# Performance work log

Measured on AMD Instinct MI355X. Metric: run time of the kernel, lower is better.

## Reference

```python
import jax, jax.numpy as jnp
import numpy as np

NUM_HEADS = 12
HEAD_DIM = 64  # d_out // num_heads = 768 // 12


def setup_inputs() -> dict:
    key = jax.random.key(0)
    k1, k2 = jax.random.split(key)
    x = jax.random.normal(k1, (2, 2048, 768), dtype=jnp.float32)
    # torch Linear weight: [d_out, d_in], y = x @ W.T
    Wq = jax.random.normal(k2, (768, 768), dtype=jnp.float32) * 0.02
    return {"x": x, "Wq": Wq}


def reference(x, Wq):
    b, n, d_in = x.shape
    H, hd = NUM_HEADS, HEAD_DIM
    d_out = H * hd
    # NOTE: the original module uses Wq for queries, keys AND values.
    qkv = x @ Wq.T                                   # [b, n, d_out]
    h = qkv.reshape(b, n, H, hd).transpose(0, 2, 1, 3)  # [b, H, n, hd]
    scores = jnp.einsum('bhqd,bhkd->bhqk', h, h)      # [b, H, n, n]
    causal = jnp.triu(jnp.ones((n, n), dtype=bool), k=1)
    scores = jnp.where(causal, -jnp.inf, scores)
    attn = jax.nn.softmax(scores / jnp.sqrt(jnp.float32(hd)), axis=-1)
    ctx = jnp.einsum('bhqk,bhkd->bhqd', attn, h)      # [b, H, n, hd]
    # faithful to source: transpose(-2,-1) -> [b, H, hd, n], then view(b, n, d_out)
    ctx = ctx.transpose(0, 1, 3, 2)
    return ctx.reshape(b, n, d_out)
```

## Files before the change

### kernel.cpp

```cpp
#include <hip/hip_runtime.h>
#include <math.h>

typedef __attribute__((ext_vector_type(8))) short  short8;
typedef __attribute__((ext_vector_type(4))) float  floatx4;
typedef __attribute__((ext_vector_type(4))) unsigned short ushort4v;

#define MFMA16(a, b, c) __builtin_amdgcn_mfma_f32_16x16x32_bf16(a, b, c, 0, 0, 0)

constexpr int NSEQ = 2048;
constexpr int DIN  = 768;
constexpr int NH   = 12;
constexpr size_t NX = (size_t)2 * NSEQ * DIN;
constexpr size_t NW = (size_t)DIN * DIN;
constexpr float QSCALE = 0.18033688011112042f;

__device__ __forceinline__ ushort f2bf(float f) {
    unsigned u = __float_as_uint(f);
    u += 0x7FFF + ((u >> 16) & 1);
    return (ushort)(u >> 16);
}
__device__ __forceinline__ float bf2f(ushort u) {
    return __uint_as_float(((unsigned)u) << 16);
}

__global__ __launch_bounds__(256)
void cvt_bf16(const float* __restrict__ x, const float* __restrict__ Wq,
              ushort* __restrict__ dst)
{
    size_t i = ((size_t)blockIdx.x * 256 + threadIdx.x) * 8;
    const float* s = (i < NX) ? (x + i) : (Wq + (i - NX));
    float4 f0 = ((const float4*)s)[0];
    float4 f1 = ((const float4*)s)[1];
    short8 o;
    o[0] = (short)f2bf(f0.x); o[1] = (short)f2bf(f0.y);
    o[2] = (short)f2bf(f0.z); o[3] = (short)f2bf(f0.w);
    o[4] = (short)f2bf(f1.x); o[5] = (short)f2bf(f1.y);
    o[6] = (short)f2bf(f1.z); o[7] = (short)f2bf(f1.w);
    *(short8*)(dst + i) = o;
}

__global__ __launch_bounds__(256, 3)
void qkv_mfma(const ushort* __restrict__ xb, const ushort* __restrict__ wb,
              ushort* __restrict__ h)
{
    __shared__ ushort As[64 * 72];
    __shared__ ushort Bs[128 * 72];

    const int tid  = threadIdx.x;
    const int w    = tid >> 6;
    const int lane = tid & 63;
    const int m    = lane & 15;
    const int quad = lane >> 4;
    const int r0   = blockIdx.x * 64;
    const int c0   = blockIdx.y * 128;
    const int mrow0 = (w & 1) * 32;
    const int ncol0 = (w >> 1) * 64;

    floatx4 C[2][4] = {};
    short8 ar[2], br[4];

    #pragma unroll
    for (int i = 0; i < 2; ++i) {
        int id = tid + i * 256;
        ar[i] = *(const short8*)(xb + (size_t)(r0 + (id >> 3)) * DIN + (id & 7) * 8);
    }
    #pragma unroll
    for (int i = 0; i < 4; ++i) {
        int id = tid + i * 256;
        br[i] = *(const short8*)(wb + (size_t)(c0 + (id >> 3)) * DIN + (id & 7) * 8);
    }

    for (int kk = 0; kk < 12; ++kk) {
        __syncthreads();
        #pragma unroll
        for (int i = 0; i < 2; ++i) {
            int id = tid + i * 256;
            *(short8*)&As[(id >> 3) * 72 + (id & 7) * 8] = ar[i];
        }
        #pragma unroll
        for (int i = 0; i < 4; ++i) {
            int id = tid + i * 256;
            *(short8*)&Bs[(id >> 3) * 72 + (id & 7) * 8] = br[i];
        }
        if (kk < 11) {
            const int k0 = (kk + 1) * 64;
            #pragma unroll
            for (int i = 0; i < 2; ++i) {
                int id = tid + i * 256;
                ar[i] = *(const short8*)(xb + (size_t)(r0 + (id >> 3)) * DIN + k0 + (id & 7) * 8);
            }
            #pragma unroll
            for (int i = 0; i < 4; ++i) {
                int id = tid + i * 256;
                br[i] = *(const short8*)(wb + (size_t)(c0 + (id >> 3)) * DIN + k0 + (id & 7) * 8);
            }
        }
        __syncthreads();

        #pragma unroll
        for (int kt2 = 0; kt2 < 2; ++kt2) {
            short8 a0 = *(const short8*)&As[(mrow0 + m)      * 72 + kt2 * 32 + quad * 8];
            short8 a1 = *(const short8*)&As[(mrow0 + 16 + m) * 72 + kt2 * 32 + quad * 8];
            #pragma unroll
            for (int nt = 0; nt < 4; ++nt) {
                short8 bf = *(const short8*)&Bs[(ncol0 + nt * 16 + m) * 72 + kt2 * 32 + quad * 8];
                C[0][nt] = MFMA16(a0, bf, C[0][nt]);
                C[1][nt] = MFMA16(a1, bf, C[1][nt]);
            }
        }
    }

    #pragma unroll
    for (int mt = 0; mt < 2; ++mt)
        #pragma unroll
        for (int nt = 0; nt < 4; ++nt) {
            int cg = c0 + ncol0 + nt * 16 + m;
            int head = cg >> 6, d = cg & 63;
            #pragma unroll
            for (int r = 0; r < 4; ++r) {
                int rg = r0 + mrow0 + mt * 16 + quad * 4 + r;
                int b = rg >> 11, q = rg & 2047;
                h[((size_t)(b * NH + head) * NSEQ + q) * 64 + d] = f2bf(C[mt][nt][r]);
            }
        }
}

__global__ __launch_bounds__(256, 4)
void attn_mfma(const ushort* __restrict__ h, float* __restrict__ out)
{
    __shared__ ushort Ks[64 * 72];
    __shared__ ushort Vt[64 * 72];
    __shared__ ushort Ps[4 * 16 * 72];

    const int tid  = threadIdx.x;
    const int w    = tid >> 6;
    const int lane = tid & 63;
    const int m    = lane & 15;
    const int quad = lane >> 4;

    const int qt = 31 - blockIdx.x;
    const int bh = blockIdx.y;
    const int q0 = qt * 64;
    const int wq = q0 + w * 16;
    const ushort* __restrict__ Hh = h + (size_t)bh * NSEQ * 64;

    short8 qa[2];
    #pragma unroll
    for (int kt2 = 0; kt2 < 2; ++kt2) {
        short8 raw = *(const short8*)(Hh + (size_t)(wq + m) * 64 + kt2 * 32 + quad * 8);
        #pragma unroll
        for (int j = 0; j < 8; ++j)
            qa[kt2][j] = (short)f2bf(bf2f((ushort)raw[j]) * QSCALE);
    }

    floatx4 O[4] = {};
    float lacc = 0.0f;
    ushort* Psw = Ps + w * 16 * 72;

    const int kr2  = (tid & 31) * 2;
    const int part = tid >> 5;
    const int nkt  = qt + 1;

    short8 a0, a1;
    {
        const ushort* src = Hh + (size_t)kr2 * 64 + part * 8;
        a0 = *(const short8*)src;
        a1 = *(const short8*)(src + 64);
    }

    for (int kt = 0; kt < nkt; ++kt) {
        __syncthreads();
        union { short8 v; ushort u[8]; } ua, ub;
        ua.v = a0; ub.v = a1;
        *(short8*)&Ks[kr2       * 72 + part * 8] = a0;
        *(short8*)&Ks[(kr2 + 1) * 72 + part * 8] = a1;
        #pragma unroll
        for (int i = 0; i < 8; ++i) {
            unsigned pk = (unsigned)ua.u[i] | ((unsigned)ub.u[i] << 16);
            *(unsigned*)&Vt[(part * 8 + i) * 72 + kr2] = pk;
        }
        if (kt + 1 < nkt) {
            const ushort* src = Hh + (size_t)((kt + 1) * 64 + kr2) * 64 + part * 8;
            a0 = *(const short8*)src;
            a1 = *(const short8*)(src + 64);
        }
        __syncthreads();

        floatx4 S[4] = {};
        #pragma unroll
        for (int kt2 = 0; kt2 < 2; ++kt2)
            #pragma unroll
            for (int mt = 0; mt < 4; ++mt) {
                short8 ka = *(const short8*)&Ks[(mt * 16 + m) * 72 + kt2 * 32 + quad * 8];
                S[mt] = MFMA16(ka, qa[kt2], S[mt]);
            }

        const int k0 = kt * 64;
        if (kt == nkt - 1) {
            #pragma unroll
            for (int mt = 0; mt < 4; ++mt) {
                ushort4v pw;
                #pragma unroll
                for (int r = 0; r < 4; ++r) {
                    int kg = k0 + mt * 16 + quad * 4 + r;
                    float p = (kg <= wq + m) ? exp2f(S[mt][r]) : 0.0f;
                    lacc += p;
                    pw[r] = f2bf(p);
                }
                *(ushort4v*)&Psw[m * 72 + mt * 16 + quad * 4] = pw;
            }
        } else {
            #pragma unroll
            for (int mt = 0; mt < 4; ++mt) {
                ushort4v pw;
                #pragma unroll
                for (int r = 0; r < 4; ++r) {
                    float p = exp2f(S[mt][r]);
                    lacc += p;
                    pw[r] = f2bf(p);
                }
                *(ushort4v*)&Psw[m * 72 + mt * 16 + quad * 4] = pw;
            }
        }

        #pragma unroll
        for (int kt2 = 0; kt2 < 2; ++kt2) {
            short8 pb = *(const short8*)&Psw[m * 72 + kt2 * 32 + quad * 8];
            #pragma unroll
            for (int mt = 0; mt < 4; ++mt) {
                short8 va = *(const short8*)&Vt[(mt * 16 + m) * 72 + kt2 * 32 + quad * 8];
                O[mt] = MFMA16(va, pb, O[mt]);
            }
        }
    }

    lacc += __shfl_xor(lacc, 16);
    lacc += __shfl_xor(lacc, 32);
    float linv = 1.0f / lacc;

    #pragma unroll
    for (int mt = 0; mt < 4; ++mt)
        #pragma unroll
        for (int r = 0; r < 4; ++r) {
            int d = mt * 16 + quad * 4 + r;
            out[((size_t)bh * 64 + d) * NSEQ + q0 + w * 16 + m] = O[mt][r] * linv;
        }
}

extern "C" void kernel_launch(void* const* d_in, const int* in_sizes, int n_in,
                              void* d_out, int out_size, void* d_ws, size_t ws_size,
                              hipStream_t stream)
{
    (void)in_sizes; (void)n_in; (void)out_size; (void)ws_size;
    const float* x  = (const float*)d_in[0];
    const float* Wq = (const float*)d_in[1];
    float* out = (float*)d_out;

    ushort* xb = (ushort*)d_ws;
    ushort* wb = xb + NX;
    ushort* hb = wb + NW;

    cvt_bf16<<<dim3((NX + NW) / (8 * 256)), dim3(256), 0, stream>>>(x, Wq, xb);
    qkv_mfma<<<dim3(64, 6), dim3(256), 0, stream>>>(xb, wb, hb);
    attn_mfma<<<dim3(32, 24), dim3(256), 0, stream>>>(hb, out);
}
```

Before: 132.1 us.

## Fuse bf16 conversion into QKV GEMM and split attention KV across chunks

Removes the standalone fp32-to-bf16 conversion kernel; the projection GEMM now loads fp32 x and Wq and converts while staging into shared memory. Attention is split along the key dimension into chunks of up to 8 tiles, giving a balanced grid of 80 blocks per head, with partial outputs written to a workspace and summed by a new combine kernel. The row-sum is computed by an extra MFMA against a ones row appended to V, and exp2 and bf16 packing use hardware intrinsics. The cost is extra partial-buffer traffic, a third launch, and more fp32 global reads in the GEMM.

```diff
diff --git a/kernel.cpp b/kernel.cpp
--- a/kernel.cpp
+++ b/kernel.cpp
@@ -1,18 +1,18 @@
 #include <hip/hip_runtime.h>
+#include <hip/hip_bf16.h>
 #include <math.h>
 
 typedef __attribute__((ext_vector_type(8))) short  short8;
 typedef __attribute__((ext_vector_type(4))) float  floatx4;
-typedef __attribute__((ext_vector_type(4))) unsigned short ushort4v;
 
 #define MFMA16(a, b, c) __builtin_amdgcn_mfma_f32_16x16x32_bf16(a, b, c, 0, 0, 0)
 
 constexpr int NSEQ = 2048;
 constexpr int DIN  = 768;
 constexpr int NH   = 12;
-constexpr size_t NX = (size_t)2 * NSEQ * DIN;
-constexpr size_t NW = (size_t)DIN * DIN;
 constexpr float QSCALE = 0.18033688011112042f;
+constexpr int PART_STRIDE = 64 * 64 + 64;
+constexpr size_t HB_ELEMS = (size_t)2 * NH * NSEQ * 64;
 
 __device__ __forceinline__ ushort f2bf(float f) {
     unsigned u = __float_as_uint(f);
@@ -22,25 +22,19 @@
 __device__ __forceinline__ float bf2f(ushort u) {
     return __uint_as_float(((unsigned)u) << 16);
 }
-
-__global__ __launch_bounds__(256)
-void cvt_bf16(const float* __restrict__ x, const float* __restrict__ Wq,
-              ushort* __restrict__ dst)
-{
-    size_t i = ((size_t)blockIdx.x * 256 + threadIdx.x) * 8;
-    const float* s = (i < NX) ? (x + i) : (Wq + (i - NX));
-    float4 f0 = ((const float4*)s)[0];
-    float4 f1 = ((const float4*)s)[1];
-    short8 o;
-    o[0] = (short)f2bf(f0.x); o[1] = (short)f2bf(f0.y);
-    o[2] = (short)f2bf(f0.z); o[3] = (short)f2bf(f0.w);
-    o[4] = (short)f2bf(f1.x); o[5] = (short)f2bf(f1.y);
-    o[6] = (short)f2bf(f1.z); o[7] = (short)f2bf(f1.w);
-    *(short8*)(dst + i) = o;
+__device__ __forceinline__ unsigned pk2(float a, float b) {
+    __hip_bfloat162 h = __float22bfloat162_rn(float2{a, b});
+    return *(unsigned*)&h;
+}
+__device__ __forceinline__ short8 cvt8(float4 a, float4 b) {
+    union { short8 s; unsigned u[4]; } r;
+    r.u[0] = pk2(a.x, a.y); r.u[1] = pk2(a.z, a.w);
+    r.u[2] = pk2(b.x, b.y); r.u[3] = pk2(b.z, b.w);
+    return r.s;
 }
 
 __global__ __launch_bounds__(256, 3)
-void qkv_mfma(const ushort* __restrict__ xb, const ushort* __restrict__ wb,
+void qkv_mfma(const float* __restrict__ x, const float* __restrict__ Wq,
               ushort* __restrict__ h)
 {
     __shared__ ushort As[64 * 72];
@@ -56,44 +50,34 @@
     const int mrow0 = (w & 1) * 32;
     const int ncol0 = (w >> 1) * 64;
 
+    const int xr = tid >> 2, xc = (tid & 3) * 16;
+    const int wr = tid >> 1, wc = (tid & 1) * 32;
+
     floatx4 C[2][4] = {};
-    short8 ar[2], br[4];
-
-    #pragma unroll
-    for (int i = 0; i < 2; ++i) {
-        int id = tid + i * 256;
-        ar[i] = *(const short8*)(xb + (size_t)(r0 + (id >> 3)) * DIN + (id & 7) * 8);
-    }
-    #pragma unroll
-    for (int i = 0; i < 4; ++i) {
-        int id = tid + i * 256;
-        br[i] = *(const short8*)(wb + (size_t)(c0 + (id >> 3)) * DIN + (id & 7) * 8);
-    }
+    float4 xa[4], wa[8];
+
+    #pragma unroll
+    for (int j = 0; j < 4; ++j)
+        xa[j] = *(const float4*)(x + (size_t)(r0 + xr) * DIN + xc + j * 4);
+    #pragma unroll
+    for (int j = 0; j < 8; ++j)
+        wa[j] = *(const float4*)(Wq + (size_t)(c0 + wr) * DIN + wc + j * 4);
 
     for (int kk = 0; kk < 12; ++kk) {
         __syncthreads();
-        #pragma unroll
-        for (int i = 0; i < 2; ++i) {
-            int id = tid + i * 256;
-            *(short8*)&As[(id >> 3) * 72 + (id & 7) * 8] = ar[i];
-        }
-        #pragma unroll
-        for (int i = 0; i < 4; ++i) {
-            int id = tid + i * 256;
-            *(short8*)&Bs[(id >> 3) * 72 + (id & 7) * 8] = br[i];
-        }
+        *(short8*)&As[xr * 72 + xc]     = cvt8(xa[0], xa[1]);
+        *(short8*)&As[xr * 72 + xc + 8] = cvt8(xa[2], xa[3]);
+        #pragma unroll
+        for (int v = 0; v < 4; ++v)
+            *(short8*)&Bs[wr * 72 + wc + v * 8] = cvt8(wa[v * 2], wa[v * 2 + 1]);
         if (kk < 11) {
             const int k0 = (kk + 1) * 64;
             #pragma unroll
-            for (int i = 0; i < 2; ++i) {
-                int id = tid + i * 256;
-                ar[i] = *(const short8*)(xb + (size_t)(r0 + (id >> 3)) * DIN + k0 + (id & 7) * 8);
-            }
-            #pragma unroll
-            for (int i = 0; i < 4; ++i) {
-                int id = tid + i * 256;
-                br[i] = *(const short8*)(wb + (size_t)(c0 + (id >> 3)) * DIN + k0 + (id & 7) * 8);
-            }
+            for (int j = 0; j < 4; ++j)
+                xa[j] = *(const float4*)(x + (size_t)(r0 + xr) * DIN + k0 + xc + j * 4);
+            #pragma unroll
+            for (int j = 0; j < 8; ++j)
+                wa[j] = *(const float4*)(Wq + (size_t)(c0 + wr) * DIN + k0 + wc + j * 4);
         }
         __syncthreads();
 
@@ -126,10 +110,11 @@
 }
 
 __global__ __launch_bounds__(256, 4)
-void attn_mfma(const ushort* __restrict__ h, float* __restrict__ out)
+void attn_mfma(const ushort* __restrict__ h, float* __restrict__ parts,
+               float* __restrict__ out)
 {
     __shared__ ushort Ks[64 * 72];
-    __shared__ ushort Vt[64 * 72];
+    __shared__ ushort Vt[80 * 72];
     __shared__ ushort Ps[4 * 16 * 72];
 
     const int tid  = threadIdx.x;
@@ -138,11 +123,21 @@
     const int m    = lane & 15;
     const int quad = lane >> 4;
 
-    const int qt = 31 - blockIdx.x;
+    const int u  = blockIdx.x;
     const int bh = blockIdx.y;
-    const int q0 = qt * 64;
-    const int wq = q0 + w * 16;
+    int qt, kc;
+    if (u < 32)      { qt = 24 + (u >> 2); kc = u & 3; }
+    else if (u < 56) { int v = u - 32; int q3 = v / 3; qt = 16 + q3; kc = v - q3 * 3; }
+    else if (u < 72) { int v = u - 56; qt = 8 + (v >> 1); kc = v & 1; }
+    else             { qt = u - 72; kc = 0; }
+    const int nc  = (qt + 8) >> 3;
+    const int kt0 = kc * 8;
+    const int kt1 = min(kc * 8 + 8, qt + 1);
+    const int q0  = qt * 64;
+    const int wq  = q0 + w * 16;
     const ushort* __restrict__ Hh = h + (size_t)bh * NSEQ * 64;
+
+    if (tid < 32) ((unsigned*)&Vt[64 * 72])[tid] = 0x3F803F80u;
 
     short8 qa[2];
     #pragma unroll
@@ -154,21 +149,20 @@
     }
 
     floatx4 O[4] = {};
-    float lacc = 0.0f;
+    floatx4 O5 = {};
     ushort* Psw = Ps + w * 16 * 72;
 
     const int kr2  = (tid & 31) * 2;
     const int part = tid >> 5;
-    const int nkt  = qt + 1;
 
     short8 a0, a1;
     {
-        const ushort* src = Hh + (size_t)kr2 * 64 + part * 8;
+        const ushort* src = Hh + (size_t)(kt0 * 64 + kr2) * 64 + part * 8;
         a0 = *(const short8*)src;
         a1 = *(const short8*)(src + 64);
     }
 
-    for (int kt = 0; kt < nkt; ++kt) {
+    for (int kt = kt0; kt < kt1; ++kt) {
         __syncthreads();
         union { short8 v; ushort u[8]; } ua, ub;
         ua.v = a0; ub.v = a1;
@@ -179,7 +173,7 @@
             unsigned pk = (unsigned)ua.u[i] | ((unsigned)ub.u[i] << 16);
             *(unsigned*)&Vt[(part * 8 + i) * 72 + kr2] = pk;
         }
-        if (kt + 1 < nkt) {
+        if (kt + 1 < kt1) {
             const ushort* src = Hh + (size_t)((kt + 1) * 64 + kr2) * 64 + part * 8;
             a0 = *(const short8*)src;
             a1 = *(const short8*)(src + 64);
@@ -195,31 +189,28 @@
                 S[mt] = MFMA16(ka, qa[kt2], S[mt]);
             }
 
-        const int k0 = kt * 64;
-        if (kt == nkt - 1) {
+        const int kb = kt * 64;
+        if (kt == qt) {
             #pragma unroll
             for (int mt = 0; mt < 4; ++mt) {
-                ushort4v pw;
+                float p[4];
                 #pragma unroll
                 for (int r = 0; r < 4; ++r) {
-                    int kg = k0 + mt * 16 + quad * 4 + r;
-                    float p = (kg <= wq + m) ? exp2f(S[mt][r]) : 0.0f;
-                    lacc += p;
-                    pw[r] = f2bf(p);
+                    int kg = kb + mt * 16 + quad * 4 + r;
+                    p[r] = (kg <= wq + m) ? __builtin_amdgcn_exp2f(S[mt][r]) : 0.0f;
                 }
-                *(ushort4v*)&Psw[m * 72 + mt * 16 + quad * 4] = pw;
+                uint2 pw = {pk2(p[0], p[1]), pk2(p[2], p[3])};
+                *(uint2*)&Psw[m * 72 + mt * 16 + quad * 4] = pw;
             }
         } else {
             #pragma unroll
             for (int mt = 0; mt < 4; ++mt) {
-                ushort4v pw;
+                float p[4];
                 #pragma unroll
-                for (int r = 0; r < 4; ++r) {
-                    float p = exp2f(S[mt][r]);
-                    lacc += p;
-                    pw[r] = f2bf(p);
-                }
-                *(ushort4v*)&Psw[m * 72 + mt * 16 + quad * 4] = pw;
+                for (int r = 0; r < 4; ++r)
+                    p[r] = __builtin_amdgcn_exp2f(S[mt][r]);
+                uint2 pw = {pk2(p[0], p[1]), pk2(p[2], p[3])};
+                *(uint2*)&Psw[m * 72 + mt * 16 + quad * 4] = pw;
             }
         }
 
@@ -231,20 +222,69 @@
                 short8 va = *(const short8*)&Vt[(mt * 16 + m) * 72 + kt2 * 32 + quad * 8];
                 O[mt] = MFMA16(va, pb, O[mt]);
             }
-        }
-    }
-
-    lacc += __shfl_xor(lacc, 16);
-    lacc += __shfl_xor(lacc, 32);
-    float linv = 1.0f / lacc;
-
-    #pragma unroll
-    for (int mt = 0; mt < 4; ++mt)
-        #pragma unroll
-        for (int r = 0; r < 4; ++r) {
-            int d = mt * 16 + quad * 4 + r;
-            out[((size_t)bh * 64 + d) * NSEQ + q0 + w * 16 + m] = O[mt][r] * linv;
-        }
+            short8 v5 = *(const short8*)&Vt[(64 + m) * 72 + kt2 * 32 + quad * 8];
+            O5 = MFMA16(v5, pb, O5);
+        }
+    }
+
+    float lval = __shfl(O5[0], m);
+
+    if (nc == 1) {
+        float linv = 1.0f / lval;
+        #pragma unroll
+        for (int mt = 0; mt < 4; ++mt)
+            #pragma unroll
+            for (int r = 0; r < 4; ++r) {
+                int d = mt * 16 + quad * 4 + r;
+                out[((size_t)bh * 64 + d) * NSEQ + q0 + w * 16 + m] = O[mt][r] * linv;
+            }
+    } else {
+        float* P = parts + (size_t)((bh * 32 + qt) * 4 + kc) * PART_STRIDE;
+        #pragma unroll
+        for (int mt = 0; mt < 4; ++mt)
+            #pragma unroll
+            for (int r = 0; r < 4; ++r)
+                P[(mt * 16 + quad * 4 + r) * 64 + w * 16 + m] = O[mt][r];
+        if (quad == 0) P[4096 + w * 16 + m] = O5[0];
+    }
+}
+
+__global__ __launch_bounds__(256)
+void combine(const float* __restrict__ parts, float* __restrict__ out)
+{
+    const int qt = 8 + blockIdx.x;
+    const int bh = blockIdx.y;
+    const int nc = (qt + 8) >> 3;
+    const float* base = parts + (size_t)((bh * 32 + qt) * 4) * PART_STRIDE;
+
+    __shared__ float linv[64];
+    const int tid = threadIdx.x;
+    if (tid < 64) {
+        float s = 0.0f;
+        for (int c = 0; c < nc; ++c) s += base[c * PART_STRIDE + 4096 + tid];
+        linv[tid] = 1.0f / s;
+    }
+    __syncthreads();
+
+    const int d  = tid >> 2;
+    const int qo = (tid & 3) * 16;
+    float4 acc[4] = {};
+    for (int c = 0; c < nc; ++c) {
+        const float4* p = (const float4*)(base + c * PART_STRIDE + d * 64 + qo);
+        #pragma unroll
+        for (int j = 0; j < 4; ++j) {
+            float4 v = p[j];
+            acc[j].x += v.x; acc[j].y += v.y; acc[j].z += v.z; acc[j].w += v.w;
+        }
+    }
+    float* dst = out + ((size_t)bh * 64 + d) * NSEQ + qt * 64 + qo;
+    #pragma unroll
+    for (int j = 0; j < 4; ++j) {
+        float4 lv = *(const float4*)&linv[qo + j * 4];
+        float4 o = make_float4(acc[j].x * lv.x, acc[j].y * lv.y,
+                               acc[j].z * lv.z, acc[j].w * lv.w);
+        *(float4*)(dst + j * 4) = o;
+    }
 }
 
 extern "C" void kernel_launch(void* const* d_in, const int* in_sizes, int n_in,
@@ -256,11 +296,10 @@
     const float* Wq = (const float*)d_in[1];
     float* out = (float*)d_out;
 
-    ushort* xb = (ushort*)d_ws;
-    ushort* wb = xb + NX;
-    ushort* hb = wb + NW;
-
-    cvt_bf16<<<dim3((NX + NW) / (8 * 256)), dim3(256), 0, stream>>>(x, Wq, xb);
-    qkv_mfma<<<dim3(64, 6), dim3(256), 0, stream>>>(xb, wb, hb);
-    attn_mfma<<<dim3(32, 24), dim3(256), 0, stream>>>(hb, out);
-}
+    ushort* hb    = (ushort*)d_ws;
+    float*  partb = (float*)((char*)d_ws + HB_ELEMS * sizeof(ushort));
+
+    qkv_mfma<<<dim3(64, 6),  dim3(256), 0, stream>>>(x, Wq, hb);
+    attn_mfma<<<dim3(80, 24), dim3(256), 0, stream>>>(hb, partb, out);
+    combine<<<dim3(24, 24),  dim3(256), 0, stream>>>(partb, out);
+}
```

Measured after the change: 136.7 us. 3.5% more time.

## Pair causal query tiles per block, drop LDS from GEMM, fold row-sum into MFMA

Applied to the files above, without the earlier changes.

The attention kernel now gives each block two query tiles (p and 31-p), which balances causal work across blocks and halves the grid. Keys are read straight from global memory instead of an LDS copy. The softmax denominator is computed by an extra MFMA against a ones row appended to the V tile, replacing the scalar accumulation and shuffles. The QKV GEMM drops shared-memory staging and loads operands directly from global, and the bf16 conversion uses the packed intrinsic. Register pressure rises and occupancy is lowered to 2, and direct global loads may increase memory traffic.

```diff
diff --git a/kernel.cpp b/kernel.cpp
--- a/kernel.cpp
+++ b/kernel.cpp
@@ -1,18 +1,19 @@
 #include <hip/hip_runtime.h>
+#include <hip/hip_bf16.h>
 #include <math.h>
 
 typedef __attribute__((ext_vector_type(8))) short  short8;
 typedef __attribute__((ext_vector_type(4))) float  floatx4;
-typedef __attribute__((ext_vector_type(4))) unsigned short ushort4v;
 
 #define MFMA16(a, b, c) __builtin_amdgcn_mfma_f32_16x16x32_bf16(a, b, c, 0, 0, 0)
 
 constexpr int NSEQ = 2048;
 constexpr int DIN  = 768;
 constexpr int NH   = 12;
+constexpr float QSCALE = 0.18033688011112042f;
 constexpr size_t NX = (size_t)2 * NSEQ * DIN;
 constexpr size_t NW = (size_t)DIN * DIN;
-constexpr float QSCALE = 0.18033688011112042f;
+constexpr size_t HB_ELEMS = (size_t)2 * NH * NSEQ * 64;
 
 __device__ __forceinline__ ushort f2bf(float f) {
     unsigned u = __float_as_uint(f);
@@ -22,6 +23,10 @@
 __device__ __forceinline__ float bf2f(ushort u) {
     return __uint_as_float(((unsigned)u) << 16);
 }
+__device__ __forceinline__ unsigned pk2(float a, float b) {
+    __hip_bfloat162 h = __float22bfloat162_rn(float2{a, b});
+    return *(unsigned*)&h;
+}
 
 __global__ __launch_bounds__(256)
 void cvt_bf16(const float* __restrict__ x, const float* __restrict__ Wq,
@@ -31,82 +36,39 @@
     const float* s = (i < NX) ? (x + i) : (Wq + (i - NX));
     float4 f0 = ((const float4*)s)[0];
     float4 f1 = ((const float4*)s)[1];
-    short8 o;
-    o[0] = (short)f2bf(f0.x); o[1] = (short)f2bf(f0.y);
-    o[2] = (short)f2bf(f0.z); o[3] = (short)f2bf(f0.w);
-    o[4] = (short)f2bf(f1.x); o[5] = (short)f2bf(f1.y);
-    o[6] = (short)f2bf(f1.z); o[7] = (short)f2bf(f1.w);
-    *(short8*)(dst + i) = o;
-}
-
-__global__ __launch_bounds__(256, 3)
+    union { short8 v; unsigned u[4]; } o;
+    o.u[0] = pk2(f0.x, f0.y); o.u[1] = pk2(f0.z, f0.w);
+    o.u[2] = pk2(f1.x, f1.y); o.u[3] = pk2(f1.z, f1.w);
+    *(short8*)(dst + i) = o.v;
+}
+
+__global__ __launch_bounds__(256, 4)
 void qkv_mfma(const ushort* __restrict__ xb, const ushort* __restrict__ wb,
               ushort* __restrict__ h)
 {
-    __shared__ ushort As[64 * 72];
-    __shared__ ushort Bs[128 * 72];
-
     const int tid  = threadIdx.x;
     const int w    = tid >> 6;
     const int lane = tid & 63;
     const int m    = lane & 15;
     const int quad = lane >> 4;
-    const int r0   = blockIdx.x * 64;
-    const int c0   = blockIdx.y * 128;
-    const int mrow0 = (w & 1) * 32;
-    const int ncol0 = (w >> 1) * 64;
+    const int wr0  = blockIdx.x * 64 + (w & 1) * 32;
+    const int wc0  = blockIdx.y * 128 + (w >> 1) * 64;
+
+    const ushort* ar0 = xb + (size_t)(wr0 + m) * DIN + quad * 8;
+    const ushort* ar1 = xb + (size_t)(wr0 + 16 + m) * DIN + quad * 8;
+    const ushort* br0 = wb + (size_t)(wc0 + m) * DIN + quad * 8;
 
     floatx4 C[2][4] = {};
-    short8 ar[2], br[4];
-
-    #pragma unroll
-    for (int i = 0; i < 2; ++i) {
-        int id = tid + i * 256;
-        ar[i] = *(const short8*)(xb + (size_t)(r0 + (id >> 3)) * DIN + (id & 7) * 8);
-    }
-    #pragma unroll
-    for (int i = 0; i < 4; ++i) {
-        int id = tid + i * 256;
-        br[i] = *(const short8*)(wb + (size_t)(c0 + (id >> 3)) * DIN + (id & 7) * 8);
-    }
-
-    for (int kk = 0; kk < 12; ++kk) {
-        __syncthreads();
-        #pragma unroll
-        for (int i = 0; i < 2; ++i) {
-            int id = tid + i * 256;
-            *(short8*)&As[(id >> 3) * 72 + (id & 7) * 8] = ar[i];
-        }
-        #pragma unroll
-        for (int i = 0; i < 4; ++i) {
-            int id = tid + i * 256;
-            *(short8*)&Bs[(id >> 3) * 72 + (id & 7) * 8] = br[i];
-        }
-        if (kk < 11) {
-            const int k0 = (kk + 1) * 64;
-            #pragma unroll
-            for (int i = 0; i < 2; ++i) {
-                int id = tid + i * 256;
-                ar[i] = *(const short8*)(xb + (size_t)(r0 + (id >> 3)) * DIN + k0 + (id & 7) * 8);
-            }
-            #pragma unroll
-            for (int i = 0; i < 4; ++i) {
-                int id = tid + i * 256;
-                br[i] = *(const short8*)(wb + (size_t)(c0 + (id >> 3)) * DIN + k0 + (id & 7) * 8);
-            }
-        }
-        __syncthreads();
-
-        #pragma unroll
-        for (int kt2 = 0; kt2 < 2; ++kt2) {
-            short8 a0 = *(const short8*)&As[(mrow0 + m)      * 72 + kt2 * 32 + quad * 8];
-            short8 a1 = *(const short8*)&As[(mrow0 + 16 + m) * 72 + kt2 * 32 + quad * 8];
-            #pragma unroll
-            for (int nt = 0; nt < 4; ++nt) {
-                short8 bf = *(const short8*)&Bs[(ncol0 + nt * 16 + m) * 72 + kt2 * 32 + quad * 8];
-                C[0][nt] = MFMA16(a0, bf, C[0][nt]);
-                C[1][nt] = MFMA16(a1, bf, C[1][nt]);
-            }
+
+    #pragma unroll 4
+    for (int k = 0; k < DIN; k += 32) {
+        short8 a0 = *(const short8*)(ar0 + k);
+        short8 a1 = *(const short8*)(ar1 + k);
+        #pragma unroll
+        for (int nt = 0; nt < 4; ++nt) {
+            short8 b = *(const short8*)(br0 + (size_t)nt * 16 * DIN + k);
+            C[0][nt] = MFMA16(a0, b, C[0][nt]);
+            C[1][nt] = MFMA16(a1, b, C[1][nt]);
         }
     }
 
@@ -114,22 +76,21 @@
     for (int mt = 0; mt < 2; ++mt)
         #pragma unroll
         for (int nt = 0; nt < 4; ++nt) {
-            int cg = c0 + ncol0 + nt * 16 + m;
+            int cg = wc0 + nt * 16 + m;
             int head = cg >> 6, d = cg & 63;
             #pragma unroll
             for (int r = 0; r < 4; ++r) {
-                int rg = r0 + mrow0 + mt * 16 + quad * 4 + r;
+                int rg = wr0 + mt * 16 + quad * 4 + r;
                 int b = rg >> 11, q = rg & 2047;
                 h[((size_t)(b * NH + head) * NSEQ + q) * 64 + d] = f2bf(C[mt][nt][r]);
             }
         }
 }
 
-__global__ __launch_bounds__(256, 4)
+__global__ __launch_bounds__(256, 2)
 void attn_mfma(const ushort* __restrict__ h, float* __restrict__ out)
 {
-    __shared__ ushort Ks[64 * 72];
-    __shared__ ushort Vt[64 * 72];
+    __shared__ ushort Vt[80 * 72];
     __shared__ ushort Ps[4 * 16 * 72];
 
     const int tid  = threadIdx.x;
@@ -138,28 +99,34 @@
     const int m    = lane & 15;
     const int quad = lane >> 4;
 
-    const int qt = 31 - blockIdx.x;
-    const int bh = blockIdx.y;
-    const int q0 = qt * 64;
-    const int wq = q0 + w * 16;
+    const int p   = blockIdx.x;
+    const int bh  = blockIdx.y;
+    const int qtA = p, qtB = 31 - p;
+    const int q0A = qtA * 64, q0B = qtB * 64;
+    const int wqA = q0A + w * 16, wqB = q0B + w * 16;
     const ushort* __restrict__ Hh = h + (size_t)bh * NSEQ * 64;
 
-    short8 qa[2];
+    for (int i = tid; i < 16 * 36; i += 256)
+        ((unsigned*)&Vt[64 * 72])[i] = (i < 36) ? 0x3F803F80u : 0u;
+
+    short8 qaA[2], qaB[2];
     #pragma unroll
     for (int kt2 = 0; kt2 < 2; ++kt2) {
-        short8 raw = *(const short8*)(Hh + (size_t)(wq + m) * 64 + kt2 * 32 + quad * 8);
-        #pragma unroll
-        for (int j = 0; j < 8; ++j)
-            qa[kt2][j] = (short)f2bf(bf2f((ushort)raw[j]) * QSCALE);
-    }
-
-    floatx4 O[4] = {};
-    float lacc = 0.0f;
+        short8 ra = *(const short8*)(Hh + (size_t)(wqA + m) * 64 + kt2 * 32 + quad * 8);
+        short8 rb = *(const short8*)(Hh + (size_t)(wqB + m) * 64 + kt2 * 32 + quad * 8);
+        #pragma unroll
+        for (int j = 0; j < 8; ++j) {
+            qaA[kt2][j] = (short)f2bf(bf2f((ushort)ra[j]) * QSCALE);
+            qaB[kt2][j] = (short)f2bf(bf2f((ushort)rb[j]) * QSCALE);
+        }
+    }
+
+    floatx4 OA[4] = {}, OB[4] = {};
+    floatx4 O5A = {}, O5B = {};
     ushort* Psw = Ps + w * 16 * 72;
 
     const int kr2  = (tid & 31) * 2;
     const int part = tid >> 5;
-    const int nkt  = qt + 1;
 
     short8 a0, a1;
     {
@@ -168,82 +135,116 @@
         a1 = *(const short8*)(src + 64);
     }
 
-    for (int kt = 0; kt < nkt; ++kt) {
+    for (int kt = 0; kt <= qtB; ++kt) {
+        const int kb = kt * 64;
         __syncthreads();
-        union { short8 v; ushort u[8]; } ua, ub;
-        ua.v = a0; ub.v = a1;
-        *(short8*)&Ks[kr2       * 72 + part * 8] = a0;
-        *(short8*)&Ks[(kr2 + 1) * 72 + part * 8] = a1;
-        #pragma unroll
-        for (int i = 0; i < 8; ++i) {
-            unsigned pk = (unsigned)ua.u[i] | ((unsigned)ub.u[i] << 16);
-            *(unsigned*)&Vt[(part * 8 + i) * 72 + kr2] = pk;
-        }
-        if (kt + 1 < nkt) {
+        {
+            union { short8 v; ushort u[8]; } ua, ub;
+            ua.v = a0; ub.v = a1;
+            #pragma unroll
+            for (int i = 0; i < 8; ++i) {
+                unsigned pkd = (unsigned)ua.u[i] | ((unsigned)ub.u[i] << 16);
+                *(unsigned*)&Vt[(part * 8 + i) * 72 + kr2] = pkd;
+            }
+        }
+        if (kt < qtB) {
             const ushort* src = Hh + (size_t)((kt + 1) * 64 + kr2) * 64 + part * 8;
             a0 = *(const short8*)src;
             a1 = *(const short8*)(src + 64);
         }
+
+        short8 ka[2][4];
+        #pragma unroll
+        for (int kt2 = 0; kt2 < 2; ++kt2)
+            #pragma unroll
+            for (int mt = 0; mt < 4; ++mt)
+                ka[kt2][mt] = *(const short8*)(Hh + (size_t)(kb + mt * 16 + m) * 64 + kt2 * 32 + quad * 8);
+
+        const bool doA = (kt <= qtA);
+
+        floatx4 SB[4] = {}, SA[4] = {};
+        #pragma unroll
+        for (int kt2 = 0; kt2 < 2; ++kt2)
+            #pragma unroll
+            for (int mt = 0; mt < 4; ++mt)
+                SB[mt] = MFMA16(ka[kt2][mt], qaB[kt2], SB[mt]);
+        if (doA)
+            #pragma unroll
+            for (int kt2 = 0; kt2 < 2; ++kt2)
+                #pragma unroll
+                for (int mt = 0; mt < 4; ++mt)
+                    SA[mt] = MFMA16(ka[kt2][mt], qaA[kt2], SA[mt]);
+
         __syncthreads();
 
-        floatx4 S[4] = {};
-        #pragma unroll
-        for (int kt2 = 0; kt2 < 2; ++kt2)
+        short8 va[2][4], v5[2];
+        #pragma unroll
+        for (int kt2 = 0; kt2 < 2; ++kt2) {
+            #pragma unroll
+            for (int mt = 0; mt < 4; ++mt)
+                va[kt2][mt] = *(const short8*)&Vt[(mt * 16 + m) * 72 + kt2 * 32 + quad * 8];
+            v5[kt2] = *(const short8*)&Vt[(64 + m) * 72 + kt2 * 32 + quad * 8];
+        }
+
+        {
+            const bool maskB = (kt == qtB);
             #pragma unroll
             for (int mt = 0; mt < 4; ++mt) {
-                short8 ka = *(const short8*)&Ks[(mt * 16 + m) * 72 + kt2 * 32 + quad * 8];
-                S[mt] = MFMA16(ka, qa[kt2], S[mt]);
-            }
-
-        const int k0 = kt * 64;
-        if (kt == nkt - 1) {
+                float pv[4];
+                #pragma unroll
+                for (int r = 0; r < 4; ++r) {
+                    int kg = kb + mt * 16 + quad * 4 + r;
+                    float e = __builtin_amdgcn_exp2f(SB[mt][r]);
+                    pv[r] = (maskB && kg > wqB + m) ? 0.0f : e;
+                }
+                uint2 pw = {pk2(pv[0], pv[1]), pk2(pv[2], pv[3])};
+                *(uint2*)&Psw[m * 72 + mt * 16 + quad * 4] = pw;
+            }
+            #pragma unroll
+            for (int kt2 = 0; kt2 < 2; ++kt2) {
+                short8 pb = *(const short8*)&Psw[m * 72 + kt2 * 32 + quad * 8];
+                #pragma unroll
+                for (int mt = 0; mt < 4; ++mt)
+                    OB[mt] = MFMA16(va[kt2][mt], pb, OB[mt]);
+                O5B = MFMA16(v5[kt2], pb, O5B);
+            }
+        }
+
+        if (doA) {
+            const bool maskA = (kt == qtA);
             #pragma unroll
             for (int mt = 0; mt < 4; ++mt) {
-                ushort4v pw;
+                float pv[4];
                 #pragma unroll
                 for (int r = 0; r < 4; ++r) {
-                    int kg = k0 + mt * 16 + quad * 4 + r;
-                    float p = (kg <= wq + m) ? exp2f(S[mt][r]) : 0.0f;
-                    lacc += p;
-                    pw[r] = f2bf(p);
+                    int kg = kb + mt * 16 + quad * 4 + r;
+                    float e = __builtin_amdgcn_exp2f(SA[mt][r]);
+                    pv[r] = (maskA && kg > wqA + m) ? 0.0f : e;
                 }
-                *(ushort4v*)&Psw[m * 72 + mt * 16 + quad * 4] = pw;
-            }
-        } else {
-            #pragma unroll
-            for (int mt = 0; mt < 4; ++mt) {
-                ushort4v pw;
-                #pragma unroll
-                for (int r = 0; r < 4; ++r) {
-                    float p = exp2f(S[mt][r]);
-                    lacc += p;
-                    pw[r] = f2bf(p);
-                }
-                *(ushort4v*)&Psw[m * 72 + mt * 16 + quad * 4] = pw;
-            }
-        }
-
-        #pragma unroll
-        for (int kt2 = 0; kt2 < 2; ++kt2) {
-            short8 pb = *(const short8*)&Psw[m * 72 + kt2 * 32 + quad * 8];
-            #pragma unroll
-            for (int mt = 0; mt < 4; ++mt) {
-                short8 va = *(const short8*)&Vt[(mt * 16 + m) * 72 + kt2 * 32 + quad * 8];
-                O[mt] = MFMA16(va, pb, O[mt]);
-            }
-        }
-    }
-
-    lacc += __shfl_xor(lacc, 16);
-    lacc += __shfl_xor(lacc, 32);
-    float linv = 1.0f / lacc;
-
+                uint2 pw = {pk2(pv[0], pv[1]), pk2(pv[2], pv[3])};
+                *(uint2*)&Psw[m * 72 + mt * 16 + quad * 4] = pw;
+            }
+            #pragma unroll
+            for (int kt2 = 0; kt2 < 2; ++kt2) {
+                short8 pb = *(const short8*)&Psw[m * 72 + kt2 * 32 + quad * 8];
+                #pragma unroll
+                for (int mt = 0; mt < 4; ++mt)
+                    OA[mt] = MFMA16(va[kt2][mt], pb, OA[mt]);
+                O5A = MFMA16(v5[kt2], pb, O5A);
+            }
+        }
+    }
+
+    float linvB = 1.0f / __shfl(O5B[0], m);
+    float linvA = 1.0f / __shfl(O5A[0], m);
     #pragma unroll
     for (int mt = 0; mt < 4; ++mt)
         #pragma unroll
         for (int r = 0; r < 4; ++r) {
             int d = mt * 16 + quad * 4 + r;
-            out[((size_t)bh * 64 + d) * NSEQ + q0 + w * 16 + m] = O[mt][r] * linv;
+            float* rowp = out + ((size_t)bh * 64 + d) * NSEQ;
+            rowp[q0B + w * 16 + m] = OB[mt][r] * linvB;
+            rowp[q0A + w * 16 + m] = OA[mt][r] * linvA;
         }
 }
 
@@ -261,6 +262,6 @@
     ushort* hb = wb + NW;
 
     cvt_bf16<<<dim3((NX + NW) / (8 * 256)), dim3(256), 0, stream>>>(x, Wq, xb);
-    qkv_mfma<<<dim3(64, 6), dim3(256), 0, stream>>>(xb, wb, hb);
-    attn_mfma<<<dim3(32, 24), dim3(256), 0, stream>>>(hb, out);
-}
+    qkv_mfma<<<dim3(64, 6),  dim3(256), 0, stream>>>(xb, wb, hb);
+    attn_mfma<<<dim3(16, 24), dim3(256), 0, stream>>>(hb, out);
+}
```

New measurement: 175.0 us. 32.5% more time.
